# Performance work log

Hardware: AMD Instinct MI355X
Metric: run time of the kernel (lower is better)

## Reference

```python
import jax, jax.numpy as jnp
import numpy as np
from jax import lax

EPS = 1e-5

def _conv(x, w, b, pad):
    y = lax.conv_general_dilated(x, w, (1, 1), [(pad, pad), (pad, pad)],
                                 dimension_numbers=('NCHW', 'OIHW', 'NCHW'))
    return y + b[None, :, None, None]

def _bn(x, g, b, m, v):
    # eval-mode BatchNorm2d with running stats
    scale = g * lax.rsqrt(v + EPS)
    return x * scale[None, :, None, None] + (b - m * scale)[None, :, None, None]

def setup_inputs() -> dict:
    key = jax.random.key(0)
    ks = jax.random.split(key, 16)
    B, C, H, W = 16, 64, 128, 128
    C2 = 2 * C
    d = {}
    d['x'] = jax.random.normal(ks[0], (B, C, H, W), jnp.float32)
    # fc1: Conv2d(C,C,3,p=1) + BN(C)
    d['fc1_w'] = jax.random.normal(ks[1], (C, C, 3, 3), jnp.float32) * 0.05
    d['fc1_b'] = jax.random.normal(ks[2], (C,), jnp.float32) * 0.05
    d['bn1_g'] = jnp.ones((C,), jnp.float32)
    d['bn1_b'] = jnp.zeros((C,), jnp.float32)
    d['bn1_m'] = jax.random.normal(ks[3], (C,), jnp.float32) * 0.05
    d['bn1_v'] = jax.random.uniform(ks[4], (C,), jnp.float32) * 0.5 + 0.5
    # graph_conv.nn: Conv2d(2C,2C,1) + BN(2C) + GELU
    d['gc_w'] = jax.random.normal(ks[5], (C2, C2, 1, 1), jnp.float32) * 0.05
    d['gc_b'] = jax.random.normal(ks[6], (C2,), jnp.float32) * 0.05
    d['bng_g'] = jnp.ones((C2,), jnp.float32)
    d['bng_b'] = jnp.zeros((C2,), jnp.float32)
    d['bng_m'] = jax.random.normal(ks[7], (C2,), jnp.float32) * 0.05
    d['bng_v'] = jax.random.uniform(ks[8], (C2,), jnp.float32) * 0.5 + 0.5
    # fc2: Conv2d(2C,C,3,p=1) + BN(C)
    d['fc2_w'] = jax.random.normal(ks[9], (C, C2, 3, 3), jnp.float32) * 0.05
    d['fc2_b'] = jax.random.normal(ks[10], (C,), jnp.float32) * 0.05
    d['bn2_g'] = jnp.ones((C,), jnp.float32)
    d['bn2_b'] = jnp.zeros((C,), jnp.float32)
    d['bn2_m'] = jax.random.normal(ks[11], (C,), jnp.float32) * 0.05
    d['bn2_v'] = jax.random.uniform(ks[12], (C,), jnp.float32) * 0.5 + 0.5
    return d

def reference(x, fc1_w, fc1_b, bn1_g, bn1_b, bn1_m, bn1_v,
              gc_w, gc_b, bng_g, bng_b, bng_m, bng_v,
              fc2_w, fc2_b, bn2_g, bn2_b, bn2_m, bn2_v):
    # fc1
    h = _bn(_conv(x, fc1_w, fc1_b, 1), bn1_g, bn1_b, bn1_m, bn1_v)
    # MRConv4dSP: strided self-attention over superpatch tokens
    sel = h[:, :, ::4, ::4]                          # [B,C,h4,w4]
    B, C, h4, w4 = sel.shape
    q = sel.reshape(B, C, h4 * w4).transpose(0, 2, 1)  # [B,N,C]
    scale = C ** (-0.5)
    att = jax.nn.softmax(jnp.einsum('bnc,bmc->bnm', q, q) * scale, axis=-1)
    o = jnp.einsum('bnm,bmc->bnc', att, q)           # [B,N,C]
    o = o.transpose(0, 2, 1).reshape(B, C, h4, w4)
    o = jnp.repeat(jnp.repeat(o, 4, axis=2), 4, axis=3)
    g = jnp.concatenate([h, o], axis=1)              # [B,2C,H,W]
    g = jax.nn.gelu(_bn(_conv(g, gc_w, gc_b, 0), bng_g, bng_b, bng_m, bng_v),
                    approximate=False)
    # fc2 + residual (drop_path=0 -> identity)
    y = _bn(_conv(g, fc2_w, fc2_b, 1), bn2_g, bn2_b, bn2_m, bn2_v)
    return y + x
```

## Files before the change

kernel.cpp:

```cpp
#include <hip/hip_runtime.h>
#include <math.h>

#define EPSV 1e-5f

typedef __bf16 bf16;
using bf16x8 = __attribute__((ext_vector_type(8))) __bf16;
using bf16x4 = __attribute__((ext_vector_type(4))) __bf16;
using bf16x2 = __attribute__((ext_vector_type(2))) __bf16;
using f32x4  = __attribute__((ext_vector_type(4))) float;

static __device__ __forceinline__ f32x4 mfma16(bf16x8 a, bf16x8 b, f32x4 c) {
    return __builtin_amdgcn_mfma_f32_16x16x32_bf16(a, b, c, 0, 0, 0);
}
static __device__ __forceinline__ f32x4 zero4() {
    f32x4 z = {0.f, 0.f, 0.f, 0.f};
    return z;
}

typedef __attribute__((address_space(1))) const char g_char_t;
typedef __attribute__((address_space(3))) char lds_char_t;
static __device__ __forceinline__ void gll16(const void* g, void* l) {
    __builtin_amdgcn_global_load_lds((g_char_t*)g, (lds_char_t*)l, 16, 0, 0);
}

static __device__ __forceinline__ float gelu_f(float v) {
    float z = fabsf(v) * 0.70710678118f;
    float t = __builtin_amdgcn_rcpf(1.f + 0.3275911f * z);
    float poly = t * (0.254829592f + t * (-0.284496736f + t * (1.421413741f +
                 t * (-1.453152027f + t * 1.061405429f))));
    float e = __expf(-z * z);
    float erfv = copysignf(1.f - poly * e, v);
    return 0.5f * v * (1.f + erfv);
}

static __device__ __forceinline__ void prep3x3_one(const float* w, bf16* wt,
                                                   int t, int CIN)
{
    int cout = t / CIN, ci = t - cout * CIN;
    int cci = ci >> 5, lg = (ci >> 3) & 3, j = ci & 7;
    int mi = cout >> 4, lix = cout & 15;
#pragma unroll
    for (int kgt = 0; kgt < 9; ++kgt) {
        float v = w[(size_t)t * 9 + kgt];
        wt[((((size_t)kgt * (CIN >> 5) + cci) * 4 + mi) * 64 + lg * 16 + lix) * 8 + j]
            = (bf16)v;
    }
}

__global__ __launch_bounds__(256) void prep_all(
    const float* __restrict__ fc1_w, const float* __restrict__ fc2_w,
    const float* __restrict__ gc_w,
    bf16* __restrict__ wt1, bf16* __restrict__ wt2, bf16* __restrict__ wtg)
{
    int bx = blockIdx.x, tid = threadIdx.x;
    if (bx < 16) {
        prep3x3_one(fc1_w, wt1, bx * 256 + tid, 64);
    } else if (bx < 48) {
        prep3x3_one(fc2_w, wt2, (bx - 16) * 256 + tid, 128);
    } else {
        int t = (bx - 48) * 256 + tid;
        int cout = t >> 7, ci = t & 127;
        int ks = ci >> 5, lg = (ci >> 3) & 3, j = ci & 7;
        wtg[(((size_t)(ks * 4 + lg) * 128) + cout) * 8 + j] = (bf16)gc_w[t];
    }
}

__global__ __launch_bounds__(256) void cvt_x_nhwc(const float* __restrict__ x,
                                                  bf16* __restrict__ xb,
                                                  float* __restrict__ zb)
{
    __shared__ float t_lds[64 * 68];
    const int bx = blockIdx.x;
    const int b  = blockIdx.y;
    const int y  = bx >> 1, x0 = (bx & 1) * 64;
    const int tid = threadIdx.x;

    if (bx == 0 && b == 0 && tid < 64)
        ((float4*)zb)[tid] = make_float4(0.f, 0.f, 0.f, 0.f);

    for (int f = tid; f < 64 * 16; f += 256) {
        int c = f >> 4, xu = f & 15;
        float4 v = *(const float4*)&x[((size_t)(b * 64 + c) << 14) + (y << 7) + x0 + xu * 4];
        t_lds[(xu * 4 + 0) * 68 + c] = v.x;
        t_lds[(xu * 4 + 1) * 68 + c] = v.y;
        t_lds[(xu * 4 + 2) * 68 + c] = v.z;
        t_lds[(xu * 4 + 3) * 68 + c] = v.w;
    }
    __syncthreads();
    for (int f = tid; f < 64 * 8; f += 256) {
        int xx = f >> 3, cu = f & 7;
        const float* p = &t_lds[xx * 68 + cu * 8];
        bf16x8 v;
#pragma unroll
        for (int j = 0; j < 8; ++j) v[j] = (bf16)p[j];
        *(bf16x8*)&xb[((size_t)((b * 128 + y) * 128) + x0 + xx) * 64 + cu * 8] = v;
    }
}

template<int CIN, int OUTMODE>
__global__ __launch_bounds__(512) void conv3x3_mfma(
    const bf16* __restrict__ in, const bf16* __restrict__ wt,
    const float* __restrict__ bias,
    const float* __restrict__ bg, const float* __restrict__ bb,
    const float* __restrict__ bm, const float* __restrict__ bv,
    const bf16* __restrict__ resid, const bf16* __restrict__ zb,
    void* __restrict__ outp)
{
    constexpr int NC = CIN >> 5;
    __shared__ bf16 in_lds[2][672 * 32];
    __shared__ bf16 w_lds[2][36 * 512];

    const int wg = blockIdx.x;
    const int v  = (wg & 7) * 64 + (wg >> 3);
    const int tile = v & 31, b = v >> 5;
    const int x0 = (tile & 1) * 64;
    const int y0 = (tile >> 1) * 8;
    const int tid  = threadIdx.x;
    const int wid  = tid >> 6;
    const int lane = tid & 63;
    const int lix  = lane & 15, lg = lane >> 4;

    int goff[6]; bool gok[6];
#pragma unroll
    for (int i = 0; i < 6; ++i) {
        int chunk = wid + 8 * i;
        int f = chunk * 64 + lane;
        int pix = f >> 2, u = f & 3;
        int sw = (pix & 3) ^ ((pix >> 2) & 3);
        int ug = u ^ sw;
        int iy = pix / 66, ix = pix - iy * 66;
        int gy = y0 + iy - 1, gx = x0 + ix - 1;
        gok[i]  = (chunk < 42) && (pix < 660) &&
                  (unsigned)gy < 128u && (unsigned)gx < 128u;
        goff[i] = ((b * 128 + gy) * 128 + gx) * CIN + ug * 8;
    }
    int rd[9];
#pragma unroll
    for (int kg = 0; kg < 3; ++kg)
#pragma unroll
        for (int t = 0; t < 3; ++t) {
            int pix0 = (wid + kg) * 66 + lix + t;
            int sw = (pix0 & 3) ^ ((pix0 >> 2) & 3);
            rd[kg * 3 + t] = pix0 * 32 + ((lg ^ sw) << 3);
        }

    f32x4 acc[4][4];
#pragma unroll
    for (int i = 0; i < 4; ++i)
#pragma unroll
        for (int j = 0; j < 4; ++j) acc[i][j] = zero4();

    auto issue_in = [&](int cci, int buf) {
#pragma unroll
        for (int i = 0; i < 6; ++i) {
            int chunk = wid + 8 * i;
            if (chunk < 42) {
                const void* src = gok[i] ? (const void*)(in + goff[i] + cci * 32)
                                         : (const void*)zb;
                gll16(src, (char*)&in_lds[buf][0] + chunk * 1024);
            }
        }
    };
    auto issue_w = [&](int cci, int buf) {
#pragma unroll
        for (int i = 0; i < 5; ++i) {
            int chunk = wid + 8 * i;
            if (chunk < 36) {
                const bf16* src = wt + ((size_t)(chunk >> 2) * NC + cci) * 2048
                                     + (chunk & 3) * 512 + lane * 8;
                gll16(src, (char*)&w_lds[buf][0] + chunk * 1024);
            }
        }
    };
    auto compute = [&](int buf) {
#pragma unroll
        for (int kgt = 0; kgt < 9; ++kgt) {
            bf16x8 af[4], bfv[4];
#pragma unroll
            for (int mi = 0; mi < 4; ++mi)
                af[mi] = *(const bf16x8*)&w_lds[buf][(kgt * 4 + mi) * 512 + lane * 8];
#pragma unroll
            for (int nj = 0; nj < 4; ++nj)
                bfv[nj] = *(const bf16x8*)&in_lds[buf][rd[kgt] + nj * 512];
            __builtin_amdgcn_s_barrier();
            asm volatile("s_waitcnt lgkmcnt(0)" ::: "memory");
            __builtin_amdgcn_sched_barrier(0);
            __builtin_amdgcn_s_setprio(1);
#pragma unroll
            for (int nj = 0; nj < 4; ++nj)
#pragma unroll
                for (int mi = 0; mi < 4; ++mi)
                    acc[mi][nj] = mfma16(af[mi], bfv[nj], acc[mi][nj]);
            __builtin_amdgcn_s_setprio(0);
            __builtin_amdgcn_sched_barrier(0);
            __builtin_amdgcn_s_barrier();
        }
    };

    issue_in(0, 0);
    issue_w(0, 0);
#pragma unroll 1
    for (int c = 0; c < NC; ++c) {
        if (c + 1 < NC) {
            issue_in(c + 1, (c + 1) & 1);
            issue_w(c + 1, (c + 1) & 1);
            if (wid < 2)      asm volatile("s_waitcnt vmcnt(11)" ::: "memory");
            else if (wid < 4) asm volatile("s_waitcnt vmcnt(10)" ::: "memory");
            else              asm volatile("s_waitcnt vmcnt(9)"  ::: "memory");
        } else {
            asm volatile("s_waitcnt vmcnt(0)" ::: "memory");
        }
        __builtin_amdgcn_s_barrier();
        __builtin_amdgcn_sched_barrier(0);
        compute(c & 1);
    }

    if (OUTMODE == 0) {
        bf16* out = (bf16*)outp;
        bf16* stg = &in_lds[0][0];
#pragma unroll
        for (int mi = 0; mi < 4; ++mi) {
            float A[4], Bc[4];
#pragma unroll
            for (int r = 0; r < 4; ++r) {
                int c = mi * 16 + lg * 4 + r;
                float s = bg[c] * rsqrtf(bv[c] + EPSV);
                A[r]  = s;
                Bc[r] = bias[c] * s + bb[c] - bm[c] * s;
            }
#pragma unroll
            for (int nj = 0; nj < 4; ++nj) {
                int px = nj * 16 + lix;
                bf16x4 vv;
#pragma unroll
                for (int r = 0; r < 4; ++r)
                    vv[r] = (bf16)(acc[mi][nj][r] * A[r] + Bc[r]);
                *(bf16x4*)&stg[(wid * 64 + px) * 68 + mi * 16 + lg * 4] = vv;
            }
        }
        __syncthreads();
#pragma unroll
        for (int k = 0; k < 8; ++k) {
            int idx = k * 512 + tid;
            int row = idx >> 9, rem = idx & 511;
            int px = rem >> 3, cu = rem & 7;
            bf16x8 vv = *(const bf16x8*)&stg[(row * 64 + px) * 68 + cu * 8];
            *(bf16x8*)&out[((size_t)((b * 128 + y0 + row) * 128)
                            + x0 + px) * 64 + cu * 8] = vv;
        }
    } else {
        float* out = (float*)outp;
        const int gy = y0 + wid;
#pragma unroll
        for (int mi = 0; mi < 4; ++mi) {
            float A[4], Bc[4];
#pragma unroll
            for (int r = 0; r < 4; ++r) {
                int c = mi * 16 + lg * 4 + r;
                float s = bg[c] * rsqrtf(bv[c] + EPSV);
                A[r]  = s;
                Bc[r] = bias[c] * s + bb[c] - bm[c] * s;
            }
#pragma unroll
            for (int nj = 0; nj < 4; ++nj) {
                int px = x0 + nj * 16 + lix;
                bf16x4 rv = *(const bf16x4*)&resid[((size_t)((b * 128 + gy) * 128) + px) * 64
                                                   + mi * 16 + lg * 4];
#pragma unroll
                for (int r = 0; r < 4; ++r) {
                    int c = mi * 16 + lg * 4 + r;
                    size_t oi = ((size_t)(b * 64 + c) << 14) + (gy << 7) + px;
                    out[oi] = acc[mi][nj][r] * A[r] + Bc[r] + (float)rv[r];
                }
            }
        }
    }
}

__global__ __launch_bounds__(256) void gather_q(const bf16* __restrict__ h,
                                                bf16* __restrict__ q)
{
    int t = blockIdx.x * 256 + threadIdx.x;
    int cu = t & 7, n = (t >> 3) & 1023, b = t >> 13;
    int y = (n >> 5) << 2, x = (n & 31) << 2;
    bf16x8 v = *(const bf16x8*)&h[((size_t)((b * 128 + y) * 128 + x)) * 64 + cu * 8];
    *(bf16x8*)&q[((size_t)(b * 1024 + n)) * 64 + cu * 8] = v;
}

__global__ __launch_bounds__(256) void attn_fused(const bf16* __restrict__ q,
                                                  bf16* __restrict__ o)
{
    __shared__ bf16 qn[64 * 72];
    __shared__ bf16 kn[128 * 72];
    __shared__ bf16 vt[64 * 136];
    __shared__ bf16 pl[4][16 * 136];
    __shared__ __align__(16) float fac[4][16];
    const int n0 = blockIdx.x * 64, b = blockIdx.y;
    const int tid = threadIdx.x, w = tid >> 6, lane = tid & 63;
    const int lix = lane & 15, lg = lane >> 4;
    const bf16* qb = q + ((size_t)b << 16);

    for (int f = tid; f < 512; f += 256) {
        int row = f >> 3, cu = f & 7;
        *(bf16x8*)&qn[row * 72 + cu * 8] =
            *(const bf16x8*)&qb[(size_t)(n0 + row) * 64 + cu * 8];
    }

    float m_run = -3.0e38f, l_run = 0.f;
    f32x4 oacc[4];
#pragma unroll
    for (int ct = 0; ct < 4; ++ct) oacc[ct] = zero4();

    for (int mt = 0; mt < 1024; mt += 128) {
        __syncthreads();
        for (int f = tid; f < 1024; f += 256) {
            int row = f >> 3, cu = f & 7;
            *(bf16x8*)&kn[row * 72 + cu * 8] =
                *(const bf16x8*)&qb[(size_t)(mt + row) * 64 + cu * 8];
        }
        for (int f = tid; f < 512; f += 256) {
            int mp = f >> 3, cu = f & 7;
            int m = mp * 2;
            bf16x8 a = *(const bf16x8*)&qb[(size_t)(mt + m) * 64 + cu * 8];
            bf16x8 c = *(const bf16x8*)&qb[(size_t)(mt + m + 1) * 64 + cu * 8];
#pragma unroll
            for (int j = 0; j < 8; ++j) {
                bf16x2 pr = {a[j], c[j]};
                *(bf16x2*)&vt[(cu * 8 + j) * 136 + m] = pr;
            }
        }
        __syncthreads();

        bf16x8 bq0 = *(const bf16x8*)&qn[(w * 16 + lix) * 72 + lg * 8];
        bf16x8 bq1 = *(const bf16x8*)&qn[(w * 16 + lix) * 72 + 32 + lg * 8];

        f32x4 s[8];
#pragma unroll
        for (int t = 0; t < 8; ++t) {
            bf16x8 a0 = *(const bf16x8*)&kn[(t * 16 + lix) * 72 + lg * 8];
            bf16x8 a1 = *(const bf16x8*)&kn[(t * 16 + lix) * 72 + 32 + lg * 8];
            s[t] = mfma16(a0, bq0, zero4());
            s[t] = mfma16(a1, bq1, s[t]);
        }

        float mx = -3.0e38f;
#pragma unroll
        for (int t = 0; t < 8; ++t)
#pragma unroll
            for (int r = 0; r < 4; ++r) { s[t][r] *= 0.125f; mx = fmaxf(mx, s[t][r]); }
        mx = fmaxf(mx, __shfl_xor(mx, 16));
        mx = fmaxf(mx, __shfl_xor(mx, 32));
        float m_new = fmaxf(m_run, mx);
        float alpha = __expf(m_run - m_new);

        float psum = 0.f;
#pragma unroll
        for (int t = 0; t < 8; ++t) {
            float p0 = __expf(s[t][0] - m_new), p1 = __expf(s[t][1] - m_new);
            float p2 = __expf(s[t][2] - m_new), p3 = __expf(s[t][3] - m_new);
            psum += (p0 + p1) + (p2 + p3);
            bf16x2 v01 = {(bf16)p0, (bf16)p1};
            bf16x2 v23 = {(bf16)p2, (bf16)p3};
            *(bf16x2*)&pl[w][lix * 136 + t * 16 + lg * 4]     = v01;
            *(bf16x2*)&pl[w][lix * 136 + t * 16 + lg * 4 + 2] = v23;
        }
        psum += __shfl_xor(psum, 16);
        psum += __shfl_xor(psum, 32);
        l_run = l_run * alpha + psum;
        m_run = m_new;
        if (lg == 0) fac[w][lix] = alpha;

        float4 a4 = *(const float4*)&fac[w][lg * 4];
        float aa[4] = {a4.x, a4.y, a4.z, a4.w};
#pragma unroll
        for (int ct = 0; ct < 4; ++ct)
#pragma unroll
            for (int r = 0; r < 4; ++r) oacc[ct][r] *= aa[r];

#pragma unroll
        for (int kk = 0; kk < 4; ++kk) {
            bf16x8 pa = *(const bf16x8*)&pl[w][lix * 136 + kk * 32 + lg * 8];
#pragma unroll
            for (int ct = 0; ct < 4; ++ct) {
                bf16x8 bv = *(const bf16x8*)&vt[(ct * 16 + lix) * 136 + kk * 32 + lg * 8];
                oacc[ct] = mfma16(pa, bv, oacc[ct]);
            }
        }
    }

    if (lg == 0) fac[w][lix] = l_run;
    float4 l4 = *(const float4*)&fac[w][lg * 4];
    float ll[4] = {1.f / l4.x, 1.f / l4.y, 1.f / l4.z, 1.f / l4.w};
#pragma unroll
    for (int ct = 0; ct < 4; ++ct)
#pragma unroll
        for (int r = 0; r < 4; ++r) {
            int n = n0 + w * 16 + lg * 4 + r;
            int c = ct * 16 + lix;
            o[((size_t)(b * 1024 + n)) * 64 + c] = (bf16)(oacc[ct][r] * ll[r]);
        }
}

__global__ __launch_bounds__(256) void conv1x1_mfma(
    const bf16* __restrict__ h, const bf16* __restrict__ ov,
    const bf16* __restrict__ wt, const float* __restrict__ bias,
    const float* __restrict__ bg, const float* __restrict__ bb,
    const float* __restrict__ bm, const float* __restrict__ bv,
    bf16* __restrict__ g)
{
    __shared__ bf16 in1[128 * 136];
    const int y = blockIdx.x, b = blockIdx.y;
    const int tid = threadIdx.x;
    const int wid = tid >> 6, lane = tid & 63;
    const int lix = lane & 15, lg = lane >> 4;
    const int wm = wid >> 1, wn = wid & 1;

    for (int f = tid; f < 128 * 16; f += 256) {
        int px = f >> 4, cu = f & 15;
        bf16x8 v;
        if (cu < 8) {
            v = *(const bf16x8*)&h[((size_t)((b * 128 + y) * 128 + px)) * 64 + cu * 8];
        } else {
            int n = ((y >> 2) << 5) + (px >> 2);
            v = *(const bf16x8*)&ov[((size_t)(b * 1024 + n)) * 64 + (cu - 8) * 8];
        }
        *(bf16x8*)&in1[px * 136 + cu * 8] = v;
    }
    __syncthreads();

    f32x4 acc[4][4];
#pragma unroll
    for (int i = 0; i < 4; ++i)
#pragma unroll
        for (int j = 0; j < 4; ++j) acc[i][j] = zero4();

#pragma unroll
    for (int ks = 0; ks < 4; ++ks) {
        bf16x8 af[4], bfv[4];
#pragma unroll
        for (int mi = 0; mi < 4; ++mi)
            af[mi] = *(const bf16x8*)&wt[(((size_t)(ks * 4 + lg) * 128) + wm * 64 + mi * 16 + lix) * 8];
#pragma unroll
        for (int nj = 0; nj < 4; ++nj)
            bfv[nj] = *(const bf16x8*)&in1[(wn * 64 + nj * 16 + lix) * 136 + ks * 32 + lg * 8];
#pragma unroll
        for (int mi = 0; mi < 4; ++mi)
#pragma unroll
            for (int nj = 0; nj < 4; ++nj)
                acc[mi][nj] = mfma16(af[mi], bfv[nj], acc[mi][nj]);
    }

    __syncthreads();
    bf16* stg = in1;
#pragma unroll
    for (int mi = 0; mi < 4; ++mi) {
        float A[4], Bc[4];
#pragma unroll
        for (int r = 0; r < 4; ++r) {
            int c = wm * 64 + mi * 16 + lg * 4 + r;
            float s = bg[c] * rsqrtf(bv[c] + EPSV);
            A[r]  = s;
            Bc[r] = bias[c] * s + bb[c] - bm[c] * s;
        }
#pragma unroll
        for (int nj = 0; nj < 4; ++nj) {
            int px = wn * 64 + nj * 16 + lix;
            bf16x4 vv;
#pragma unroll
            for (int r = 0; r < 4; ++r)
                vv[r] = (bf16)gelu_f(acc[mi][nj][r] * A[r] + Bc[r]);
            *(bf16x4*)&stg[px * 132 + wm * 64 + mi * 16 + lg * 4] = vv;
        }
    }
    __syncthreads();
#pragma unroll
    for (int k = 0; k < 8; ++k) {
        int idx = k * 256 + tid;
        int px = idx >> 4, cu = idx & 15;
        bf16x8 v = *(const bf16x8*)&stg[px * 132 + cu * 8];
        *(bf16x8*)&g[((size_t)((b * 128 + y) * 128) + px) * 128 + cu * 8] = v;
    }
}

extern "C" void kernel_launch(void* const* d_in, const int* in_sizes, int n_in,
                              void* d_out, int out_size, void* d_ws, size_t ws_size,
                              hipStream_t stream)
{
    const float* x     = (const float*)d_in[0];
    const float* fc1_w = (const float*)d_in[1];
    const float* fc1_b = (const float*)d_in[2];
    const float* bn1_g = (const float*)d_in[3];
    const float* bn1_b = (const float*)d_in[4];
    const float* bn1_m = (const float*)d_in[5];
    const float* bn1_v = (const float*)d_in[6];
    const float* gc_w  = (const float*)d_in[7];
    const float* gc_b  = (const float*)d_in[8];
    const float* bng_g = (const float*)d_in[9];
    const float* bng_b = (const float*)d_in[10];
    const float* bng_m = (const float*)d_in[11];
    const float* bng_v = (const float*)d_in[12];
    const float* fc2_w = (const float*)d_in[13];
    const float* fc2_b = (const float*)d_in[14];
    const float* bn2_g = (const float*)d_in[15];
    const float* bn2_b = (const float*)d_in[16];
    const float* bn2_m = (const float*)d_in[17];
    const float* bn2_v = (const float*)d_in[18];

    char* wsb = (char*)d_ws;
    bf16* x_bf = (bf16*)wsb;
    bf16* h    = (bf16*)(wsb + 33554432);
    bf16* g    = (bf16*)(wsb + 67108864);
    bf16* q    = (bf16*)(wsb + 134217728);
    bf16* o    = (bf16*)(wsb + 136314880);
    bf16* wt1  = (bf16*)(wsb + 138412032);
    bf16* wt2  = (bf16*)(wsb + 138485760);
    bf16* wtg  = (bf16*)(wsb + 138633216);
    bf16* zb   = (bf16*)(wsb + 138665984);

    prep_all<<<112, 256, 0, stream>>>(fc1_w, fc2_w, gc_w, wt1, wt2, wtg);

    cvt_x_nhwc<<<dim3(256, 16), 256, 0, stream>>>(x, x_bf, (float*)zb);

    conv3x3_mfma<64, 0><<<512, 512, 0, stream>>>(
        x_bf, wt1, fc1_b, bn1_g, bn1_b, bn1_m, bn1_v, nullptr, zb, h);

    gather_q<<<512, 256, 0, stream>>>(h, q);

    attn_fused<<<dim3(16, 16), 256, 0, stream>>>(q, o);

    conv1x1_mfma<<<dim3(128, 16), 256, 0, stream>>>(
        h, o, wtg, gc_b, bng_g, bng_b, bng_m, bng_v, g);

    conv3x3_mfma<128, 1><<<512, 512, 0, stream>>>(
        g, wt2, fc2_b, bn2_g, bn2_b, bn2_m, bn2_v, x_bf, zb, (float*)d_out);
}
```

Before: 188.4 us.

## Fuse NCHW fp32 input conversion and q gather into conv3x3, double-buffer fragments

The conv3x3 kernel gains an input mode that reads fp32 NCHW x directly through registers, converts it to bf16 and stages it into LDS. This removes the separate cvt_x_nhwc kernel and its bf16 copy of x. The fc1 epilogue also writes the strided q tokens, which removes the gather_q launch, and fc2 reads the fp32 residual straight from x. The compute loop now prefetches the next kernel tap's LDS fragments while the current MFMAs run, replacing the per-tap barriers and setprio. The trade-off is that the fused input path uses strided scalar global loads with a full vmcnt(0) wait, so it overlaps less than the old async direct-to-LDS path.

```diff
diff --git a/kernel.cpp b/kernel.cpp
--- a/kernel.cpp
+++ b/kernel.cpp
@@ -50,7 +50,8 @@
 __global__ __launch_bounds__(256) void prep_all(
     const float* __restrict__ fc1_w, const float* __restrict__ fc2_w,
     const float* __restrict__ gc_w,
-    bf16* __restrict__ wt1, bf16* __restrict__ wt2, bf16* __restrict__ wtg)
+    bf16* __restrict__ wt1, bf16* __restrict__ wt2, bf16* __restrict__ wtg,
+    float* __restrict__ zb)
 {
     int bx = blockIdx.x, tid = threadIdx.x;
     if (bx < 16) {
@@ -58,6 +59,8 @@
     } else if (bx < 48) {
         prep3x3_one(fc2_w, wt2, (bx - 16) * 256 + tid, 128);
     } else {
+        if (bx == 48 && tid < 64)
+            ((float4*)zb)[tid] = make_float4(0.f, 0.f, 0.f, 0.f);
         int t = (bx - 48) * 256 + tid;
         int cout = t >> 7, ci = t & 127;
         int ks = ci >> 5, lg = (ci >> 3) & 3, j = ci & 7;
@@ -65,46 +68,14 @@
     }
 }
 
-__global__ __launch_bounds__(256) void cvt_x_nhwc(const float* __restrict__ x,
-                                                  bf16* __restrict__ xb,
-                                                  float* __restrict__ zb)
-{
-    __shared__ float t_lds[64 * 68];
-    const int bx = blockIdx.x;
-    const int b  = blockIdx.y;
-    const int y  = bx >> 1, x0 = (bx & 1) * 64;
-    const int tid = threadIdx.x;
-
-    if (bx == 0 && b == 0 && tid < 64)
-        ((float4*)zb)[tid] = make_float4(0.f, 0.f, 0.f, 0.f);
-
-    for (int f = tid; f < 64 * 16; f += 256) {
-        int c = f >> 4, xu = f & 15;
-        float4 v = *(const float4*)&x[((size_t)(b * 64 + c) << 14) + (y << 7) + x0 + xu * 4];
-        t_lds[(xu * 4 + 0) * 68 + c] = v.x;
-        t_lds[(xu * 4 + 1) * 68 + c] = v.y;
-        t_lds[(xu * 4 + 2) * 68 + c] = v.z;
-        t_lds[(xu * 4 + 3) * 68 + c] = v.w;
-    }
-    __syncthreads();
-    for (int f = tid; f < 64 * 8; f += 256) {
-        int xx = f >> 3, cu = f & 7;
-        const float* p = &t_lds[xx * 68 + cu * 8];
-        bf16x8 v;
-#pragma unroll
-        for (int j = 0; j < 8; ++j) v[j] = (bf16)p[j];
-        *(bf16x8*)&xb[((size_t)((b * 128 + y) * 128) + x0 + xx) * 64 + cu * 8] = v;
-    }
-}
-
-template<int CIN, int OUTMODE>
+template<int CIN, int INMODE, int OUTMODE>
 __global__ __launch_bounds__(512) void conv3x3_mfma(
-    const bf16* __restrict__ in, const bf16* __restrict__ wt,
+    const void* __restrict__ inp, const bf16* __restrict__ wt,
     const float* __restrict__ bias,
     const float* __restrict__ bg, const float* __restrict__ bb,
     const float* __restrict__ bm, const float* __restrict__ bv,
-    const bf16* __restrict__ resid, const bf16* __restrict__ zb,
-    void* __restrict__ outp)
+    const float* __restrict__ xres, const bf16* __restrict__ zb,
+    void* __restrict__ outp, bf16* __restrict__ qout)
 {
     constexpr int NC = CIN >> 5;
     __shared__ bf16 in_lds[2][672 * 32];
@@ -120,7 +91,7 @@
     const int lane = tid & 63;
     const int lix  = lane & 15, lg = lane >> 4;
 
-    int goff[6]; bool gok[6];
+    size_t goff[6]; bool gok[6];
 #pragma unroll
     for (int i = 0; i < 6; ++i) {
         int chunk = wid + 8 * i;
@@ -132,7 +103,10 @@
         int gy = y0 + iy - 1, gx = x0 + ix - 1;
         gok[i]  = (chunk < 42) && (pix < 660) &&
                   (unsigned)gy < 128u && (unsigned)gx < 128u;
-        goff[i] = ((b * 128 + gy) * 128 + gx) * CIN + ug * 8;
+        if (INMODE == 0)
+            goff[i] = (size_t)((b * 128 + gy) * 128 + gx) * CIN + ug * 8;
+        else
+            goff[i] = ((size_t)(b * CIN + ug * 8) << 14) + (gy << 7) + gx;
     }
     int rd[9];
 #pragma unroll
@@ -150,14 +124,40 @@
 #pragma unroll
         for (int j = 0; j < 4; ++j) acc[i][j] = zero4();
 
+    const bf16* inb = (const bf16*)inp;
+    const float* inf = (const float*)inp;
+    float fr[6][8];
+
     auto issue_in = [&](int cci, int buf) {
 #pragma unroll
         for (int i = 0; i < 6; ++i) {
             int chunk = wid + 8 * i;
             if (chunk < 42) {
-                const void* src = gok[i] ? (const void*)(in + goff[i] + cci * 32)
+                const void* src = gok[i] ? (const void*)(inb + goff[i] + cci * 32)
                                          : (const void*)zb;
                 gll16(src, (char*)&in_lds[buf][0] + chunk * 1024);
+            }
+        }
+    };
+    auto stage_load = [&](int cci) {
+#pragma unroll
+        for (int i = 0; i < 6; ++i) {
+#pragma unroll
+            for (int j = 0; j < 8; ++j)
+                fr[i][j] = gok[i]
+                    ? inf[goff[i] + ((size_t)cci << 19) + ((size_t)j << 14)]
+                    : 0.f;
+        }
+    };
+    auto stage_write = [&](int buf) {
+#pragma unroll
+        for (int i = 0; i < 6; ++i) {
+            int chunk = wid + 8 * i;
+            if (chunk < 42) {
+                bf16x8 vv;
+#pragma unroll
+                for (int j = 0; j < 8; ++j) vv[j] = (bf16)fr[i][j];
+                *(bf16x8*)&in_lds[buf][chunk * 512 + lane * 8] = vv;
             }
         }
     };
@@ -173,46 +173,74 @@
         }
     };
     auto compute = [&](int buf) {
+        bf16x8 afA[4], bfA[4], afB[4], bfB[4];
+#pragma unroll
+        for (int mi = 0; mi < 4; ++mi)
+            afA[mi] = *(const bf16x8*)&w_lds[buf][(0 * 4 + mi) * 512 + lane * 8];
+#pragma unroll
+        for (int nj = 0; nj < 4; ++nj)
+            bfA[nj] = *(const bf16x8*)&in_lds[buf][rd[0] + nj * 512];
 #pragma unroll
         for (int kgt = 0; kgt < 9; ++kgt) {
-            bf16x8 af[4], bfv[4];
-#pragma unroll
-            for (int mi = 0; mi < 4; ++mi)
-                af[mi] = *(const bf16x8*)&w_lds[buf][(kgt * 4 + mi) * 512 + lane * 8];
+            bf16x8* afC = (kgt & 1) ? afB : afA;
+            bf16x8* bfC = (kgt & 1) ? bfB : bfA;
+            bf16x8* afN = (kgt & 1) ? afA : afB;
+            bf16x8* bfN = (kgt & 1) ? bfA : bfB;
+            if (kgt < 8) {
+#pragma unroll
+                for (int mi = 0; mi < 4; ++mi)
+                    afN[mi] = *(const bf16x8*)&w_lds[buf][((kgt + 1) * 4 + mi) * 512 + lane * 8];
+#pragma unroll
+                for (int nj = 0; nj < 4; ++nj)
+                    bfN[nj] = *(const bf16x8*)&in_lds[buf][rd[kgt + 1] + nj * 512];
+            }
+            __builtin_amdgcn_sched_barrier(0);
 #pragma unroll
             for (int nj = 0; nj < 4; ++nj)
-                bfv[nj] = *(const bf16x8*)&in_lds[buf][rd[kgt] + nj * 512];
+#pragma unroll
+                for (int mi = 0; mi < 4; ++mi)
+                    acc[mi][nj] = mfma16(afC[mi], bfC[nj], acc[mi][nj]);
+            __builtin_amdgcn_sched_barrier(0);
+        }
+    };
+
+    if constexpr (INMODE == 0) {
+        issue_in(0, 0);
+        issue_w(0, 0);
+#pragma unroll 1
+        for (int c = 0; c < NC; ++c) {
+            if (c + 1 < NC) {
+                issue_in(c + 1, (c + 1) & 1);
+                issue_w(c + 1, (c + 1) & 1);
+                if (wid < 2)      asm volatile("s_waitcnt vmcnt(11)" ::: "memory");
+                else if (wid < 4) asm volatile("s_waitcnt vmcnt(10)" ::: "memory");
+                else              asm volatile("s_waitcnt vmcnt(9)"  ::: "memory");
+            } else {
+                asm volatile("s_waitcnt vmcnt(0)" ::: "memory");
+            }
             __builtin_amdgcn_s_barrier();
+            __builtin_amdgcn_sched_barrier(0);
+            compute(c & 1);
+            __builtin_amdgcn_s_barrier();
+        }
+    } else {
+        stage_load(0);
+        stage_write(0);
+        issue_w(0, 0);
+#pragma unroll 1
+        for (int c = 0; c < NC; ++c) {
+            if (c + 1 < NC) {
+                issue_w(c + 1, (c + 1) & 1);
+                stage_load(c + 1);
+            }
+            asm volatile("s_waitcnt vmcnt(0)" ::: "memory");
             asm volatile("s_waitcnt lgkmcnt(0)" ::: "memory");
+            __builtin_amdgcn_s_barrier();
             __builtin_amdgcn_sched_barrier(0);
-            __builtin_amdgcn_s_setprio(1);
-#pragma unroll
-            for (int nj = 0; nj < 4; ++nj)
-#pragma unroll
-                for (int mi = 0; mi < 4; ++mi)
-                    acc[mi][nj] = mfma16(af[mi], bfv[nj], acc[mi][nj]);
-            __builtin_amdgcn_s_setprio(0);
-            __builtin_amdgcn_sched_barrier(0);
+            compute(c & 1);
+            if (c + 1 < NC) stage_write((c + 1) & 1);
             __builtin_amdgcn_s_barrier();
         }
-    };
-
-    issue_in(0, 0);
-    issue_w(0, 0);
-#pragma unroll 1
-    for (int c = 0; c < NC; ++c) {
-        if (c + 1 < NC) {
-            issue_in(c + 1, (c + 1) & 1);
-            issue_w(c + 1, (c + 1) & 1);
-            if (wid < 2)      asm volatile("s_waitcnt vmcnt(11)" ::: "memory");
-            else if (wid < 4) asm volatile("s_waitcnt vmcnt(10)" ::: "memory");
-            else              asm volatile("s_waitcnt vmcnt(9)"  ::: "memory");
-        } else {
-            asm volatile("s_waitcnt vmcnt(0)" ::: "memory");
-        }
-        __builtin_amdgcn_s_barrier();
-        __builtin_amdgcn_sched_barrier(0);
-        compute(c & 1);
     }
 
     if (OUTMODE == 0) {
@@ -248,6 +276,15 @@
             *(bf16x8*)&out[((size_t)((b * 128 + y0 + row) * 128)
                             + x0 + px) * 64 + cu * 8] = vv;
         }
+        if (qout && tid < 256) {
+            int row4 = (tid >> 7) * 4;
+            int rem  = tid & 127;
+            int px4  = (rem >> 3) * 4, cu = rem & 7;
+            int gy = y0 + row4, gx = x0 + px4;
+            int n = ((gy >> 2) << 5) + (gx >> 2);
+            bf16x8 vv = *(const bf16x8*)&stg[(row4 * 64 + px4) * 68 + cu * 8];
+            *(bf16x8*)&qout[((size_t)(b * 1024 + n)) * 64 + cu * 8] = vv;
+        }
     } else {
         float* out = (float*)outp;
         const int gy = y0 + wid;
@@ -264,27 +301,15 @@
 #pragma unroll
             for (int nj = 0; nj < 4; ++nj) {
                 int px = x0 + nj * 16 + lix;
-                bf16x4 rv = *(const bf16x4*)&resid[((size_t)((b * 128 + gy) * 128) + px) * 64
-                                                   + mi * 16 + lg * 4];
 #pragma unroll
                 for (int r = 0; r < 4; ++r) {
                     int c = mi * 16 + lg * 4 + r;
                     size_t oi = ((size_t)(b * 64 + c) << 14) + (gy << 7) + px;
-                    out[oi] = acc[mi][nj][r] * A[r] + Bc[r] + (float)rv[r];
+                    out[oi] = acc[mi][nj][r] * A[r] + Bc[r] + xres[oi];
                 }
             }
         }
     }
-}
-
-__global__ __launch_bounds__(256) void gather_q(const bf16* __restrict__ h,
-                                                bf16* __restrict__ q)
-{
-    int t = blockIdx.x * 256 + threadIdx.x;
-    int cu = t & 7, n = (t >> 3) & 1023, b = t >> 13;
-    int y = (n >> 5) << 2, x = (n & 31) << 2;
-    bf16x8 v = *(const bf16x8*)&h[((size_t)((b * 128 + y) * 128 + x)) * 64 + cu * 8];
-    *(bf16x8*)&q[((size_t)(b * 1024 + n)) * 64 + cu * 8] = v;
 }
 
 __global__ __launch_bounds__(256) void attn_fused(const bf16* __restrict__ q,
@@ -507,30 +532,26 @@
     const float* bn2_v = (const float*)d_in[18];
 
     char* wsb = (char*)d_ws;
-    bf16* x_bf = (bf16*)wsb;
-    bf16* h    = (bf16*)(wsb + 33554432);
-    bf16* g    = (bf16*)(wsb + 67108864);
-    bf16* q    = (bf16*)(wsb + 134217728);
-    bf16* o    = (bf16*)(wsb + 136314880);
-    bf16* wt1  = (bf16*)(wsb + 138412032);
-    bf16* wt2  = (bf16*)(wsb + 138485760);
-    bf16* wtg  = (bf16*)(wsb + 138633216);
-    bf16* zb   = (bf16*)(wsb + 138665984);
-
-    prep_all<<<112, 256, 0, stream>>>(fc1_w, fc2_w, gc_w, wt1, wt2, wtg);
-
-    cvt_x_nhwc<<<dim3(256, 16), 256, 0, stream>>>(x, x_bf, (float*)zb);
-
-    conv3x3_mfma<64, 0><<<512, 512, 0, stream>>>(
-        x_bf, wt1, fc1_b, bn1_g, bn1_b, bn1_m, bn1_v, nullptr, zb, h);
-
-    gather_q<<<512, 256, 0, stream>>>(h, q);
+    bf16* h    = (bf16*)wsb;
+    bf16* g    = (bf16*)(wsb + 33554432);
+    bf16* q    = (bf16*)(wsb + 100663296);
+    bf16* o    = (bf16*)(wsb + 102760448);
+    bf16* wt1  = (bf16*)(wsb + 104857600);
+    bf16* wt2  = (bf16*)(wsb + 104931328);
+    bf16* wtg  = (bf16*)(wsb + 105078784);
+    bf16* zb   = (bf16*)(wsb + 105111552);
+
+    prep_all<<<112, 256, 0, stream>>>(fc1_w, fc2_w, gc_w, wt1, wt2, wtg,
+                                      (float*)zb);
+
+    conv3x3_mfma<64, 1, 0><<<512, 512, 0, stream>>>(
+        x, wt1, fc1_b, bn1_g, bn1_b, bn1_m, bn1_v, nullptr, zb, h, q);
 
     attn_fused<<<dim3(16, 16), 256, 0, stream>>>(q, o);
 
     conv1x1_mfma<<<dim3(128, 16), 256, 0, stream>>>(
         h, o, wtg, gc_b, bng_g, bng_b, bng_m, bng_v, g);
 
-    conv3x3_mfma<128, 1><<<512, 512, 0, stream>>>(
-        g, wt2, fc2_b, bn2_g, bn2_b, bn2_m, bn2_v, x_bf, zb, (float*)d_out);
-}
+    conv3x3_mfma<128, 0, 1><<<512, 512, 0, stream>>>(
+        g, wt2, fc2_b, bn2_g, bn2_b, bn2_m, bn2_v, x, zb, (float*)d_out, nullptr);
+}
```

Result: slower. 194.1 us (+3.0%).

## Double-buffer LDS fragments in conv3x3 and fuse q gather into conv epilogue

Applied to the files above, without the earlier changes.

The conv3x3 inner loop now prefetches the next tap's weight and input fragments from LDS into a second register set while the current tap's MFMAs run. This removes the two per-tap barriers and the lgkmcnt wait, keeping one barrier per channel chunk. The strided q gather is folded into the fc1 conv epilogue from the staging LDS, which drops the gather_q launch. Zeroing of the zero buffer moves to prep_all. The extra fragment registers raise VGPR pressure.

```diff
diff --git a/kernel.cpp b/kernel.cpp
--- a/kernel.cpp
+++ b/kernel.cpp
@@ -50,7 +50,8 @@
 __global__ __launch_bounds__(256) void prep_all(
     const float* __restrict__ fc1_w, const float* __restrict__ fc2_w,
     const float* __restrict__ gc_w,
-    bf16* __restrict__ wt1, bf16* __restrict__ wt2, bf16* __restrict__ wtg)
+    bf16* __restrict__ wt1, bf16* __restrict__ wt2, bf16* __restrict__ wtg,
+    float* __restrict__ zb)
 {
     int bx = blockIdx.x, tid = threadIdx.x;
     if (bx < 16) {
@@ -58,6 +59,8 @@
     } else if (bx < 48) {
         prep3x3_one(fc2_w, wt2, (bx - 16) * 256 + tid, 128);
     } else {
+        if (bx == 48 && tid < 64)
+            ((float4*)zb)[tid] = make_float4(0.f, 0.f, 0.f, 0.f);
         int t = (bx - 48) * 256 + tid;
         int cout = t >> 7, ci = t & 127;
         int ks = ci >> 5, lg = (ci >> 3) & 3, j = ci & 7;
@@ -66,17 +69,13 @@
 }
 
 __global__ __launch_bounds__(256) void cvt_x_nhwc(const float* __restrict__ x,
-                                                  bf16* __restrict__ xb,
-                                                  float* __restrict__ zb)
+                                                  bf16* __restrict__ xb)
 {
     __shared__ float t_lds[64 * 68];
     const int bx = blockIdx.x;
     const int b  = blockIdx.y;
     const int y  = bx >> 1, x0 = (bx & 1) * 64;
     const int tid = threadIdx.x;
-
-    if (bx == 0 && b == 0 && tid < 64)
-        ((float4*)zb)[tid] = make_float4(0.f, 0.f, 0.f, 0.f);
 
     for (int f = tid; f < 64 * 16; f += 256) {
         int c = f >> 4, xu = f & 15;
@@ -104,7 +103,7 @@
     const float* __restrict__ bg, const float* __restrict__ bb,
     const float* __restrict__ bm, const float* __restrict__ bv,
     const bf16* __restrict__ resid, const bf16* __restrict__ zb,
-    void* __restrict__ outp)
+    void* __restrict__ outp, bf16* __restrict__ qout)
 {
     constexpr int NC = CIN >> 5;
     __shared__ bf16 in_lds[2][672 * 32];
@@ -173,27 +172,34 @@
         }
     };
     auto compute = [&](int buf) {
+        bf16x8 afA[4], bfA[4], afB[4], bfB[4];
+#pragma unroll
+        for (int mi = 0; mi < 4; ++mi)
+            afA[mi] = *(const bf16x8*)&w_lds[buf][(0 * 4 + mi) * 512 + lane * 8];
+#pragma unroll
+        for (int nj = 0; nj < 4; ++nj)
+            bfA[nj] = *(const bf16x8*)&in_lds[buf][rd[0] + nj * 512];
 #pragma unroll
         for (int kgt = 0; kgt < 9; ++kgt) {
-            bf16x8 af[4], bfv[4];
-#pragma unroll
-            for (int mi = 0; mi < 4; ++mi)
-                af[mi] = *(const bf16x8*)&w_lds[buf][(kgt * 4 + mi) * 512 + lane * 8];
+            bf16x8* afC = (kgt & 1) ? afB : afA;
+            bf16x8* bfC = (kgt & 1) ? bfB : bfA;
+            bf16x8* afN = (kgt & 1) ? afA : afB;
+            bf16x8* bfN = (kgt & 1) ? bfA : bfB;
+            if (kgt < 8) {
+#pragma unroll
+                for (int mi = 0; mi < 4; ++mi)
+                    afN[mi] = *(const bf16x8*)&w_lds[buf][((kgt + 1) * 4 + mi) * 512 + lane * 8];
+#pragma unroll
+                for (int nj = 0; nj < 4; ++nj)
+                    bfN[nj] = *(const bf16x8*)&in_lds[buf][rd[kgt + 1] + nj * 512];
+            }
+            __builtin_amdgcn_sched_barrier(0);
 #pragma unroll
             for (int nj = 0; nj < 4; ++nj)
-                bfv[nj] = *(const bf16x8*)&in_lds[buf][rd[kgt] + nj * 512];
-            __builtin_amdgcn_s_barrier();
-            asm volatile("s_waitcnt lgkmcnt(0)" ::: "memory");
+#pragma unroll
+                for (int mi = 0; mi < 4; ++mi)
+                    acc[mi][nj] = mfma16(afC[mi], bfC[nj], acc[mi][nj]);
             __builtin_amdgcn_sched_barrier(0);
-            __builtin_amdgcn_s_setprio(1);
-#pragma unroll
-            for (int nj = 0; nj < 4; ++nj)
-#pragma unroll
-                for (int mi = 0; mi < 4; ++mi)
-                    acc[mi][nj] = mfma16(af[mi], bfv[nj], acc[mi][nj]);
-            __builtin_amdgcn_s_setprio(0);
-            __builtin_amdgcn_sched_barrier(0);
-            __builtin_amdgcn_s_barrier();
         }
     };
 
@@ -213,6 +219,7 @@
         __builtin_amdgcn_s_barrier();
         __builtin_amdgcn_sched_barrier(0);
         compute(c & 1);
+        __builtin_amdgcn_s_barrier();
     }
 
     if (OUTMODE == 0) {
@@ -248,6 +255,15 @@
             *(bf16x8*)&out[((size_t)((b * 128 + y0 + row) * 128)
                             + x0 + px) * 64 + cu * 8] = vv;
         }
+        if (qout && tid < 256) {
+            int row4 = (tid >> 7) * 4;
+            int rem  = tid & 127;
+            int px4  = (rem >> 3) * 4, cu = rem & 7;
+            int gy = y0 + row4, gx = x0 + px4;
+            int n = ((gy >> 2) << 5) + (gx >> 2);
+            bf16x8 vv = *(const bf16x8*)&stg[(row4 * 64 + px4) * 68 + cu * 8];
+            *(bf16x8*)&qout[((size_t)(b * 1024 + n)) * 64 + cu * 8] = vv;
+        }
     } else {
         float* out = (float*)outp;
         const int gy = y0 + wid;
@@ -275,16 +291,6 @@
             }
         }
     }
-}
-
-__global__ __launch_bounds__(256) void gather_q(const bf16* __restrict__ h,
-                                                bf16* __restrict__ q)
-{
-    int t = blockIdx.x * 256 + threadIdx.x;
-    int cu = t & 7, n = (t >> 3) & 1023, b = t >> 13;
-    int y = (n >> 5) << 2, x = (n & 31) << 2;
-    bf16x8 v = *(const bf16x8*)&h[((size_t)((b * 128 + y) * 128 + x)) * 64 + cu * 8];
-    *(bf16x8*)&q[((size_t)(b * 1024 + n)) * 64 + cu * 8] = v;
 }
 
 __global__ __launch_bounds__(256) void attn_fused(const bf16* __restrict__ q,
@@ -517,14 +523,13 @@
     bf16* wtg  = (bf16*)(wsb + 138633216);
     bf16* zb   = (bf16*)(wsb + 138665984);
 
-    prep_all<<<112, 256, 0, stream>>>(fc1_w, fc2_w, gc_w, wt1, wt2, wtg);
-
-    cvt_x_nhwc<<<dim3(256, 16), 256, 0, stream>>>(x, x_bf, (float*)zb);
+    prep_all<<<112, 256, 0, stream>>>(fc1_w, fc2_w, gc_w, wt1, wt2, wtg,
+                                      (float*)zb);
+
+    cvt_x_nhwc<<<dim3(256, 16), 256, 0, stream>>>(x, x_bf);
 
     conv3x3_mfma<64, 0><<<512, 512, 0, stream>>>(
-        x_bf, wt1, fc1_b, bn1_g, bn1_b, bn1_m, bn1_v, nullptr, zb, h);
-
-    gather_q<<<512, 256, 0, stream>>>(h, q);
+        x_bf, wt1, fc1_b, bn1_g, bn1_b, bn1_m, bn1_v, nullptr, zb, h, q);
 
     attn_fused<<<dim3(16, 16), 256, 0, stream>>>(q, o);
 
@@ -532,5 +537,5 @@
         h, o, wtg, gc_b, bng_g, bng_b, bng_m, bng_v, g);
 
     conv3x3_mfma<128, 1><<<512, 512, 0, stream>>>(
-        g, wt2, fc2_b, bn2_g, bn2_b, bn2_m, bn2_v, x_bf, zb, (float*)d_out);
-}
+        g, wt2, fc2_b, bn2_g, bn2_b, bn2_m, bn2_v, x_bf, zb, (float*)d_out, nullptr);
+}
```

Measured after the change: 179.4 us. 4.8% less time.
